# Kernel optimization log

Measured on AMD Instinct MI355X. Metric: run time of the kernel, lower is better.

Reference implementation:

```python
import jax, jax.numpy as jnp
import numpy as np

B, S, D, N, L, V = 2, 512, 1024, 4096, 4, 32000
EPS = 1e-5

def ternarize(w):
    # BitNet b1.58-style: scale = mean |w|, quantize to {-1,0,1}, rescale.
    s = jnp.mean(jnp.abs(w)) + 1e-8
    return s * jnp.round(jnp.clip(w / s, -1.0, 1.0))

def tern_ste(w):
    # straight-through estimator (faithful to ternary training)
    return w + jax.lax.stop_gradient(ternarize(w) - w)

def layer_norm(x, g, b):
    mu = jnp.mean(x, axis=-1, keepdims=True)
    var = jnp.var(x, axis=-1, keepdims=True)
    return (x - mu) * jax.lax.rsqrt(var + EPS) * g + b

def setup_inputs() -> dict:
    key = jax.random.key(0)
    ks = jax.random.split(key, 20)
    sc = lambda d: 1.0 / np.sqrt(d)
    inp = {
        'input_ids': jax.random.randint(ks[0], (B, S), 0, V, dtype=jnp.int32),
        'emb':       jax.random.normal(ks[1], (V, D), jnp.float32) * 0.02,
        'pos_emb':   jax.random.normal(ks[2], (S, D), jnp.float32) * 0.02,
        'gru_wih':   jax.random.normal(ks[3], (3 * D, D), jnp.float32) * sc(D),
        'gru_whh':   jax.random.normal(ks[4], (3 * D, D), jnp.float32) * sc(D),
        'gru_bih':   jnp.zeros((3 * D,), jnp.float32),
        'gru_bhh':   jnp.zeros((3 * D,), jnp.float32),
        'syn_w':     jax.random.normal(ks[5], (L, N, D), jnp.float32) * sc(D),
        'syn_b':     jnp.zeros((L, N), jnp.float32),
        'out_w':     jax.random.normal(ks[6], (L, D, N), jnp.float32) * sc(N),
        'out_b':     jnp.zeros((L, D), jnp.float32),
        'ln_g':      jnp.ones((L, D), jnp.float32),
        'ln_b':      jnp.zeros((L, D), jnp.float32),
        'on_g':      jnp.ones((D,), jnp.float32),
        'on_b':      jnp.zeros((D,), jnp.float32),
        'head_w':    jax.random.normal(ks[7], (V, D), jnp.float32) * sc(D),
        'head_b':    jnp.zeros((V,), jnp.float32),
    }
    return inp

def gru(x, wih, whh, bih, bhh):
    # x: [B,S,D] -> [B,S,D], torch nn.GRU semantics, h0 = 0
    # Precompute input projections for all timesteps: [B,S,3D]
    gi_all = jnp.einsum('bsd,ed->bse', x, wih) + bih
    def step(h, gi):
        gh = h @ whh.T + bhh
        ir, iz, inn = jnp.split(gi, 3, axis=-1)
        hr, hz, hn = jnp.split(gh, 3, axis=-1)
        r = jax.nn.sigmoid(ir + hr)
        z = jax.nn.sigmoid(iz + hz)
        n = jnp.tanh(inn + r * hn)
        h_new = (1.0 - z) * n + z * h
        return h_new, h_new
    h0 = jnp.zeros((x.shape[0], whh.shape[1]), x.dtype)
    _, hs = jax.lax.scan(step, h0, jnp.swapaxes(gi_all, 0, 1))
    return jnp.swapaxes(hs, 0, 1)

def reference(input_ids, emb, pos_emb, gru_wih, gru_whh, gru_bih, gru_bhh,
              syn_w, syn_b, out_w, out_b, ln_g, ln_b, on_g, on_b,
              head_w, head_b):
    # Ternary embedding lookup
    x = tern_ste(emb)[input_ids]                       # [B,S,D]
    x = x + pos_emb[None, :x.shape[1], :]
    x = gru(x, gru_wih, gru_whh, gru_bih, gru_bhh)
    for l in range(L):
        residual = x
        hidden = jax.nn.relu(jnp.einsum('bsd,nd->bsn', x, tern_ste(syn_w[l])) + syn_b[l])
        out = jnp.einsum('bsn,dn->bsd', hidden, tern_ste(out_w[l])) + out_b[l]
        x = layer_norm(residual + out, ln_g[l], ln_b[l])
    x = layer_norm(x, on_g, on_b)
    logits = jnp.einsum('bsd,vd->bsv', x, tern_ste(head_w)) + head_b  # [B,S,V]
    return logits
```

## Files before the change

kernel.cpp:

```cpp
#include <hip/hip_runtime.h>
#include <hip/hip_bf16.h>
#include <cstdint>
#include <cstddef>

#define Dm 1024
#define Sm 512
#define Bm 2
#define Nm 4096
#define Lm 4
#define Vm 32000

typedef __attribute__((ext_vector_type(8))) short short8;
typedef __attribute__((ext_vector_type(4))) float floatx4;

__device__ __forceinline__ unsigned short f2b(float f){
  union { float f; unsigned u; } v; v.f = f;
  unsigned r = (v.u + 0x7fffu + ((v.u >> 16) & 1u)) >> 16;
  return (unsigned short)r;
}

__device__ __forceinline__ float tern_thresh(double s64){
  float T = (float)(s64 * 0.5);
  if ((double)T > s64 * 0.5) T = __uint_as_float(__float_as_uint(T) - 1u);
  return T;
}

__global__ __launch_bounds__(256) void absum_part_kernel(
    const float* __restrict__ x, long n4, double* __restrict__ part)
{
  long i = (long)blockIdx.x * blockDim.x + threadIdx.x;
  long stride = (long)gridDim.x * blockDim.x;
  double s = 0.0;
  for (; i < n4; i += stride){
    float4 v = ((const float4*)x)[i];
    s += (double)fabsf(v.x) + (double)fabsf(v.y)
       + (double)fabsf(v.z) + (double)fabsf(v.w);
  }
  #pragma unroll
  for (int off = 32; off; off >>= 1) s += __shfl_down(s, off, 64);
  __shared__ double wsum[4];
  int lane = threadIdx.x & 63, wv = threadIdx.x >> 6;
  if (lane == 0) wsum[wv] = s;
  __syncthreads();
  if (threadIdx.x == 0) part[blockIdx.x] = wsum[0]+wsum[1]+wsum[2]+wsum[3];
}

__global__ __launch_bounds__(256) void absum_final_kernel(
    const double* __restrict__ part, double* __restrict__ scales)
{
  const double* p = part + (size_t)blockIdx.x * 512;
  int tid = threadIdx.x;
  double s = p[tid] + p[tid + 256];
  #pragma unroll
  for (int off = 32; off; off >>= 1) s += __shfl_down(s, off, 64);
  __shared__ double wsum[4];
  int lane = tid & 63, wv = tid >> 6;
  if (lane == 0) wsum[wv] = s;
  __syncthreads();
  if (tid == 0) scales[blockIdx.x] = wsum[0]+wsum[1]+wsum[2]+wsum[3];
}

__global__ __launch_bounds__(256) void pack_kernel(
    const float* __restrict__ src, unsigned short* __restrict__ dst, long n4,
    const double* __restrict__ ssum, double cnt)
{
  float T = 0.f;
  bool tern = (ssum != nullptr);
  if (tern){
    double s64 = ssum[0] / cnt + 1e-8;
    T = tern_thresh(s64);
  }
  long i = (long)blockIdx.x * blockDim.x + threadIdx.x;
  long stride = (long)gridDim.x * blockDim.x;
  for (; i < n4; i += stride){
    float4 v = ((const float4*)src)[i];
    ushort4 u;
    if (tern){
      u.x = (v.x > T) ? 0x3F80 : ((v.x < -T) ? 0xBF80 : 0);
      u.y = (v.y > T) ? 0x3F80 : ((v.y < -T) ? 0xBF80 : 0);
      u.z = (v.z > T) ? 0x3F80 : ((v.z < -T) ? 0xBF80 : 0);
      u.w = (v.w > T) ? 0x3F80 : ((v.w < -T) ? 0xBF80 : 0);
    } else {
      u.x = f2b(v.x); u.y = f2b(v.y); u.z = f2b(v.z); u.w = f2b(v.w);
    }
    ((ushort4*)dst)[i] = u;
  }
}

__global__ __launch_bounds__(256) void embed_kernel(
    const int* __restrict__ ids, const float* __restrict__ emb,
    const float* __restrict__ pos, const double* __restrict__ ssum,
    unsigned short* __restrict__ xb)
{
  int row = blockIdx.x;
  int sp  = row & (Sm - 1);
  int id  = ids[row];
  double s64 = ssum[0] / ((double)Vm * (double)Dm) + 1e-8;
  float s = (float)s64;
  float T = tern_thresh(s64);
  int d = threadIdx.x * 4;
  float4 wv = *(const float4*)(emb + (size_t)id * Dm + d);
  float4 pv = *(const float4*)(pos + (size_t)sp * Dm + d);
  float q0 = (wv.x > T) ? 1.f : ((wv.x < -T) ? -1.f : 0.f);
  float q1 = (wv.y > T) ? 1.f : ((wv.y < -T) ? -1.f : 0.f);
  float q2 = (wv.z > T) ? 1.f : ((wv.z < -T) ? -1.f : 0.f);
  float q3 = (wv.w > T) ? 1.f : ((wv.w < -T) ? -1.f : 0.f);
  float y0 = s * q0 + pv.x;
  float y1 = s * q1 + pv.y;
  float y2 = s * q2 + pv.z;
  float y3 = s * q3 + pv.w;
  ushort4 u = make_ushort4(f2b(y0), f2b(y1), f2b(y2), f2b(y3));
  *(ushort4*)(xb + (size_t)row * Dm + d) = u;
}

template<int WM>
__global__ __launch_bounds__(256) void gemm_t(
    const unsigned short* __restrict__ A, const void* __restrict__ Wp,
    const float* __restrict__ bias, const double* __restrict__ ssum, double cnt,
    int relu, float* __restrict__ outf, unsigned short* __restrict__ outb,
    int M, int N, int K)
{
  __shared__ unsigned short As[128][40];
  __shared__ unsigned short Bs[128][40];
  int tid = threadIdx.x;
  int wave = tid >> 6, lane = tid & 63;
  int wm = wave >> 1, wn = wave & 1;
  int bm = blockIdx.y, bn = blockIdx.x;

  float s = 1.f, T = 0.f;
  if (ssum){
    double s64 = ssum[0] / cnt + 1e-8;
    s = (float)s64;
    T = tern_thresh(s64);
  }

  int arow = tid >> 1, achunk = tid & 1;
  const unsigned short* Ag = A + (size_t)(bm * 128 + arow) * K + achunk * 16;
  const float* Wg32 = (const float*)Wp + (size_t)(bn * 128 + arow) * K + achunk * 16;
  const unsigned short* Wg16 = (const unsigned short*)Wp + (size_t)(bn * 128 + arow) * K + achunk * 16;

  floatx4 acc[4][4];
  #pragma unroll
  for (int i = 0; i < 4; i++)
    #pragma unroll
    for (int j = 0; j < 4; j++)
      acc[i][j] = (floatx4){0.f, 0.f, 0.f, 0.f};

  for (int k0 = 0; k0 < K; k0 += 32){
    __syncthreads();
    uint4 a0 = *(const uint4*)(Ag + k0);
    uint4 a1 = *(const uint4*)(Ag + k0 + 8);
    *(uint4*)&As[arow][achunk * 16]     = a0;
    *(uint4*)&As[arow][achunk * 16 + 8] = a1;
    if (WM == 2){
      uint4 b0 = *(const uint4*)(Wg16 + k0);
      uint4 b1 = *(const uint4*)(Wg16 + k0 + 8);
      *(uint4*)&Bs[arow][achunk * 16]     = b0;
      *(uint4*)&Bs[arow][achunk * 16 + 8] = b1;
    } else {
      unsigned short tmp[16];
      #pragma unroll
      for (int q = 0; q < 4; q++){
        float4 wv = *(const float4*)(Wg32 + k0 + q * 4);
        if (WM == 1){
          tmp[q*4+0] = (wv.x > T) ? 0x3F80 : ((wv.x < -T) ? 0xBF80 : 0);
          tmp[q*4+1] = (wv.y > T) ? 0x3F80 : ((wv.y < -T) ? 0xBF80 : 0);
          tmp[q*4+2] = (wv.z > T) ? 0x3F80 : ((wv.z < -T) ? 0xBF80 : 0);
          tmp[q*4+3] = (wv.w > T) ? 0x3F80 : ((wv.w < -T) ? 0xBF80 : 0);
        } else {
          tmp[q*4+0] = f2b(wv.x); tmp[q*4+1] = f2b(wv.y);
          tmp[q*4+2] = f2b(wv.z); tmp[q*4+3] = f2b(wv.w);
        }
      }
      *(uint4*)&Bs[arow][achunk * 16]     = *(uint4*)&tmp[0];
      *(uint4*)&Bs[arow][achunk * 16 + 8] = *(uint4*)&tmp[8];
    }
    __syncthreads();

    int kq = lane >> 4, mr = lane & 15;
    short8 af[4], bf[4];
    #pragma unroll
    for (int i = 0; i < 4; i++) af[i] = *(const short8*)&As[wm*64 + i*16 + mr][kq*8];
    #pragma unroll
    for (int j = 0; j < 4; j++) bf[j] = *(const short8*)&Bs[wn*64 + j*16 + mr][kq*8];
    #pragma unroll
    for (int i = 0; i < 4; i++)
      #pragma unroll
      for (int j = 0; j < 4; j++)
        acc[i][j] = __builtin_amdgcn_mfma_f32_16x16x32_bf16(af[i], bf[j], acc[i][j], 0, 0, 0);
  }

  int cr = lane >> 4, cc = lane & 15;
  #pragma unroll
  for (int j = 0; j < 4; j++){
    int col = bn * 128 + wn * 64 + j * 16 + cc;
    float bv = bias ? bias[col] : 0.f;
    #pragma unroll
    for (int i = 0; i < 4; i++){
      #pragma unroll
      for (int r = 0; r < 4; r++){
        int row = bm * 128 + wm * 64 + i * 16 + cr * 4 + r;
        float v = acc[i][j][r] * s + bv;
        if (relu) v = fmaxf(v, 0.f);
        size_t idx = (size_t)row * N + col;
        if (outf) outf[idx] = v;
        if (outb) outb[idx] = f2b(v);
      }
    }
  }
}

template<int WM>
__global__ __launch_bounds__(512) void gemm256_t(
    const unsigned short* __restrict__ A, const void* __restrict__ Wp,
    const float* __restrict__ bias, const double* __restrict__ ssum, double cnt,
    int relu, float* __restrict__ outf, unsigned short* __restrict__ outb,
    int M, int N, int K)
{
  __shared__ unsigned short As[256][40];
  __shared__ unsigned short Bs[128][40];
  int tid = threadIdx.x;
  int wave = tid >> 6, lane = tid & 63;
  int wm = wave >> 1, wn = wave & 1;
  int bm = blockIdx.y, bn = blockIdx.x;

  float s = 1.f, T = 0.f;
  if (ssum){
    double s64 = ssum[0] / cnt + 1e-8;
    s = (float)s64;
    T = tern_thresh(s64);
  }

  int arow = tid >> 1, achunk = tid & 1;
  int wrow = tid >> 2, wchunk = tid & 3;
  const unsigned short* Ag = A + (size_t)(bm * 256 + arow) * K + achunk * 16;
  const float* Wg32 = (const float*)Wp + (size_t)(bn * 128 + wrow) * K + wchunk * 8;
  const unsigned short* Wg16 = (const unsigned short*)Wp + (size_t)(bn * 128 + wrow) * K + wchunk * 8;

  floatx4 acc[4][4];
  #pragma unroll
  for (int i = 0; i < 4; i++)
    #pragma unroll
    for (int j = 0; j < 4; j++)
      acc[i][j] = (floatx4){0.f, 0.f, 0.f, 0.f};

  for (int k0 = 0; k0 < K; k0 += 32){
    __syncthreads();
    uint4 a0 = *(const uint4*)(Ag + k0);
    uint4 a1 = *(const uint4*)(Ag + k0 + 8);
    *(uint4*)&As[arow][achunk * 16]     = a0;
    *(uint4*)&As[arow][achunk * 16 + 8] = a1;
    if (WM == 2){
      uint4 b0 = *(const uint4*)(Wg16 + k0);
      *(uint4*)&Bs[wrow][wchunk * 8] = b0;
    } else {
      unsigned short tmp[8];
      float4 w0 = *(const float4*)(Wg32 + k0);
      float4 w1 = *(const float4*)(Wg32 + k0 + 4);
      if (WM == 1){
        tmp[0] = (w0.x > T) ? 0x3F80 : ((w0.x < -T) ? 0xBF80 : 0);
        tmp[1] = (w0.y > T) ? 0x3F80 : ((w0.y < -T) ? 0xBF80 : 0);
        tmp[2] = (w0.z > T) ? 0x3F80 : ((w0.z < -T) ? 0xBF80 : 0);
        tmp[3] = (w0.w > T) ? 0x3F80 : ((w0.w < -T) ? 0xBF80 : 0);
        tmp[4] = (w1.x > T) ? 0x3F80 : ((w1.x < -T) ? 0xBF80 : 0);
        tmp[5] = (w1.y > T) ? 0x3F80 : ((w1.y < -T) ? 0xBF80 : 0);
        tmp[6] = (w1.z > T) ? 0x3F80 : ((w1.z < -T) ? 0xBF80 : 0);
        tmp[7] = (w1.w > T) ? 0x3F80 : ((w1.w < -T) ? 0xBF80 : 0);
      } else {
        tmp[0] = f2b(w0.x); tmp[1] = f2b(w0.y); tmp[2] = f2b(w0.z); tmp[3] = f2b(w0.w);
        tmp[4] = f2b(w1.x); tmp[5] = f2b(w1.y); tmp[6] = f2b(w1.z); tmp[7] = f2b(w1.w);
      }
      *(uint2*)&Bs[wrow][wchunk * 8]     = *(uint2*)&tmp[0];
      *(uint2*)&Bs[wrow][wchunk * 8 + 4] = *(uint2*)&tmp[4];
    }
    __syncthreads();

    int kq = lane >> 4, mr = lane & 15;
    short8 af[4], bf[4];
    #pragma unroll
    for (int i = 0; i < 4; i++) af[i] = *(const short8*)&As[wm*64 + i*16 + mr][kq*8];
    #pragma unroll
    for (int j = 0; j < 4; j++) bf[j] = *(const short8*)&Bs[wn*64 + j*16 + mr][kq*8];
    #pragma unroll
    for (int i = 0; i < 4; i++)
      #pragma unroll
      for (int j = 0; j < 4; j++)
        acc[i][j] = __builtin_amdgcn_mfma_f32_16x16x32_bf16(af[i], bf[j], acc[i][j], 0, 0, 0);
  }

  int cr = lane >> 4, cc = lane & 15;
  #pragma unroll
  for (int j = 0; j < 4; j++){
    int col = bn * 128 + wn * 64 + j * 16 + cc;
    float bv = bias ? bias[col] : 0.f;
    #pragma unroll
    for (int i = 0; i < 4; i++){
      #pragma unroll
      for (int r = 0; r < 4; r++){
        int row = bm * 256 + wm * 64 + i * 16 + cr * 4 + r;
        float v = acc[i][j][r] * s + bv;
        if (relu) v = fmaxf(v, 0.f);
        size_t idx = (size_t)row * N + col;
        if (outf) outf[idx] = v;
        if (outb) outb[idx] = f2b(v);
      }
    }
  }
}

__global__ __launch_bounds__(512) void gru_kernel(
    const float* __restrict__ gi, const float* __restrict__ whh, const float* __restrict__ bhh,
    unsigned long long* __restrict__ hbuf,
    float* __restrict__ hs, unsigned short* __restrict__ hsb)
{
  __shared__ __align__(16) float lds_h[2][Dm];
  __shared__ float lds_gh[24];
  int w = blockIdx.x, tid = threadIdx.x;
  int bb = w & 1, slice = w >> 1;
  int d0 = slice * 8;
  int o = tid >> 4, c = tid & 15;
  bool active = (o < 24);
  int g = o >> 3, dl = o & 7;
  int wrow = g * Dm + d0 + dl;
  float4 wr0 = {0,0,0,0}, wr1 = wr0, wr2 = wr0, wr3 = wr0,
         wr4 = wr0, wr5 = wr0, wr6 = wr0, wr7 = wr0,
         wr8 = wr0, wr9 = wr0, wr10 = wr0, wr11 = wr0,
         wr12 = wr0, wr13 = wr0, wr14 = wr0, wr15 = wr0;
  if (active){
    const float* wsrc = whh + (size_t)wrow * Dm + c * 4;
    wr0  = *(const float4*)(wsrc +  0*64);  wr1  = *(const float4*)(wsrc +  1*64);
    wr2  = *(const float4*)(wsrc +  2*64);  wr3  = *(const float4*)(wsrc +  3*64);
    wr4  = *(const float4*)(wsrc +  4*64);  wr5  = *(const float4*)(wsrc +  5*64);
    wr6  = *(const float4*)(wsrc +  6*64);  wr7  = *(const float4*)(wsrc +  7*64);
    wr8  = *(const float4*)(wsrc +  8*64);  wr9  = *(const float4*)(wsrc +  9*64);
    wr10 = *(const float4*)(wsrc + 10*64);  wr11 = *(const float4*)(wsrc + 11*64);
    wr12 = *(const float4*)(wsrc + 12*64);  wr13 = *(const float4*)(wsrc + 13*64);
    wr14 = *(const float4*)(wsrc + 14*64);  wr15 = *(const float4*)(wsrc + 15*64);
  }
  float bhval = (active && c == 0) ? bhh[wrow] : 0.f;

  int gidx = tid * 2;
  bool self = ((tid >> 2) == slice);
  int dd = tid;
  int dth = d0 + (tid & 7);
  float pir = 0.f, piz = 0.f, pin = 0.f;
  if (tid < 8){
    const float* girow = gi + (size_t)bb * Sm * (3 * Dm);
    pir = girow[dth]; piz = girow[Dm + dth]; pin = girow[2*Dm + dth];
  }

  for (int t = 0; t < Sm; t++){
    float* lh = lds_h[t & 1];
    if (!self || t == 0){
      const unsigned long long* hsrc = hbuf + (size_t)(t & 1) * 2048 + bb * 1024 + gidx;
      unsigned long long e0, e1;
      int spins = 0;
      for (;;){
        e0 = __hip_atomic_load(hsrc + 0, __ATOMIC_RELAXED, __HIP_MEMORY_SCOPE_AGENT);
        e1 = __hip_atomic_load(hsrc + 1, __ATOMIC_RELAXED, __HIP_MEMORY_SCOPE_AGENT);
        if (((unsigned)(e0 >> 32) == (unsigned)t) &&
            ((unsigned)(e1 >> 32) == (unsigned)t)) break;
        __builtin_amdgcn_s_sleep(2);
        if (++spins > (1 << 16)) break;
      }
      lh[gidx + 0] = __uint_as_float((unsigned)e0);
      lh[gidx + 1] = __uint_as_float((unsigned)e1);
    }
    __syncthreads();
    float acc = 0.f;
    if (active){
      const float* hb = lh + c * 4;
      float4 hv;
      #define GDOT(J, W) hv = *(const float4*)(hb + (J)*64); \
          acc += W.x*hv.x + W.y*hv.y + W.z*hv.z + W.w*hv.w;
      GDOT(0,wr0)  GDOT(1,wr1)  GDOT(2,wr2)  GDOT(3,wr3)
      GDOT(4,wr4)  GDOT(5,wr5)  GDOT(6,wr6)  GDOT(7,wr7)
      GDOT(8,wr8)  GDOT(9,wr9)  GDOT(10,wr10) GDOT(11,wr11)
      GDOT(12,wr12) GDOT(13,wr13) GDOT(14,wr14) GDOT(15,wr15)
      #undef GDOT
    }
    #pragma unroll
    for (int off = 8; off; off >>= 1) acc += __shfl_xor(acc, off, 16);
    if (active && c == 0) lds_gh[o] = acc + bhval;
    __syncthreads();
    if (tid < 8){
      float gr = lds_gh[dd];
      float gz = lds_gh[8 + dd];
      float gn = lds_gh[16 + dd];
      float hv = lh[dth];
      float rr = 1.f / (1.f + expf(-(pir + gr)));
      float zz = 1.f / (1.f + expf(-(piz + gz)));
      float nn = tanhf(pin + rr * gn);
      float hnew = (1.f - zz) * nn + zz * hv;
      unsigned long long pack =
          ((unsigned long long)(unsigned)(t + 1) << 32) | (unsigned long long)__float_as_uint(hnew);
      __hip_atomic_store(hbuf + (size_t)((t + 1) & 1) * 2048 + bb * 1024 + dth, pack,
                         __ATOMIC_RELAXED, __HIP_MEMORY_SCOPE_AGENT);
      lds_h[(t + 1) & 1][dth] = hnew;
      if (t + 1 < Sm){
        const float* girow = gi + ((size_t)bb * Sm + (t+1)) * (3 * Dm);
        pir = girow[dth]; piz = girow[Dm + dth]; pin = girow[2*Dm + dth];
      }
      size_t oi = ((size_t)bb * Sm + t) * Dm + dth;
      hs[oi]  = hnew;
      hsb[oi] = f2b(hnew);
    }
  }
}

__global__ __launch_bounds__(256) void ln_kernel(
    float* __restrict__ resid, const float* __restrict__ addv,
    const float* __restrict__ g, const float* __restrict__ b,
    float* __restrict__ outf, unsigned short* __restrict__ outb)
{
  int row = blockIdx.x;
  int d = threadIdx.x * 4;
  size_t base = (size_t)row * Dm + d;
  float4 v = *(float4*)(resid + base);
  if (addv){
    float4 a = *(const float4*)(addv + base);
    v.x += a.x; v.y += a.y; v.z += a.z; v.w += a.w;
  }
  float sum = v.x + v.y + v.z + v.w;
  float sq  = v.x*v.x + v.y*v.y + v.z*v.z + v.w*v.w;
  #pragma unroll
  for (int off = 32; off; off >>= 1){
    sum += __shfl_down(sum, off, 64);
    sq  += __shfl_down(sq,  off, 64);
  }
  __shared__ float red[4][2];
  __shared__ float bc[2];
  int lane = threadIdx.x & 63, wv = threadIdx.x >> 6;
  if (lane == 0){ red[wv][0] = sum; red[wv][1] = sq; }
  __syncthreads();
  if (threadIdx.x == 0){
    float st = red[0][0] + red[1][0] + red[2][0] + red[3][0];
    float qt = red[0][1] + red[1][1] + red[2][1] + red[3][1];
    float mu = st * (1.f / Dm);
    float var = qt * (1.f / Dm) - mu * mu;
    bc[0] = mu; bc[1] = rsqrtf(var + 1e-5f);
  }
  __syncthreads();
  float mu = bc[0], rs = bc[1];
  float4 gv = *(const float4*)(g + d);
  float4 bv = *(const float4*)(b + d);
  float4 y;
  y.x = (v.x - mu) * rs * gv.x + bv.x;
  y.y = (v.y - mu) * rs * gv.y + bv.y;
  y.z = (v.z - mu) * rs * gv.z + bv.z;
  y.w = (v.w - mu) * rs * gv.w + bv.w;
  if (outf) *(float4*)(outf + base) = y;
  if (outb){
    ushort4 u = make_ushort4(f2b(y.x), f2b(y.y), f2b(y.z), f2b(y.w));
    *(ushort4*)(outb + base) = u;
  }
}

extern "C" void kernel_launch(void* const* d_in, const int* in_sizes, int n_in,
                              void* d_out, int out_size, void* d_ws, size_t ws_size,
                              hipStream_t stream)
{
  const int*   ids    = (const int*)  d_in[0];
  const float* emb    = (const float*)d_in[1];
  const float* pos    = (const float*)d_in[2];
  const float* wih    = (const float*)d_in[3];
  const float* whh    = (const float*)d_in[4];
  const float* bih    = (const float*)d_in[5];
  const float* bhh    = (const float*)d_in[6];
  const float* syn_w  = (const float*)d_in[7];
  const float* syn_b  = (const float*)d_in[8];
  const float* out_w  = (const float*)d_in[9];
  const float* out_b  = (const float*)d_in[10];
  const float* ln_g   = (const float*)d_in[11];
  const float* ln_b   = (const float*)d_in[12];
  const float* on_g   = (const float*)d_in[13];
  const float* on_b   = (const float*)d_in[14];
  const float* head_w = (const float*)d_in[15];
  const float* head_b = (const float*)d_in[16];
  float* logits = (float*)d_out;

  char* ws = (char*)d_ws;
  double*             scales = (double*)ws;
  unsigned long long* hbuf   = (unsigned long long*)(ws + 4096);
  double*             parts  = (double*)(ws + 36864);
  unsigned short*     xb     = (unsigned short*)(ws + 131072);
  float*              hs     = (float*)(ws + ((size_t)4  << 20));
  unsigned short*     hidden = (unsigned short*)(ws + ((size_t)12 << 20));
  float*              outbuf = (float*)(ws + ((size_t)20 << 20));
  float*              gi     = (float*)(ws + ((size_t)24 << 20));
  unsigned short*     wih_b  = (unsigned short*)(ws + ((size_t)36 << 20));
  unsigned short*     syn_bk = (unsigned short*)(ws + ((size_t)42 << 20));
  unsigned short*     out_bk = (unsigned short*)(ws + ((size_t)74 << 20));
  unsigned short*     head_bk= (unsigned short*)(ws + ((size_t)106 << 20));
  const size_t NEED = ((size_t)106 << 20) + (size_t)Vm * Dm * 2;
  const bool packed = (ws_size >= NEED);

  hipMemsetAsync(d_ws, 0, 36864, stream);

  {
    long n;
    n = (long)Vm * Dm;
    absum_part_kernel<<<512, 256, 0, stream>>>(emb, n / 4, parts + 0 * 512);
    for (int l = 0; l < Lm; l++){
      n = (long)Nm * Dm;
      absum_part_kernel<<<512, 256, 0, stream>>>(syn_w + (size_t)l * Nm * Dm, n / 4, parts + (size_t)(1 + l) * 512);
      absum_part_kernel<<<512, 256, 0, stream>>>(out_w + (size_t)l * Dm * Nm, n / 4, parts + (size_t)(5 + l) * 512);
    }
    n = (long)Vm * Dm;
    absum_part_kernel<<<512, 256, 0, stream>>>(head_w, n / 4, parts + 9 * 512);
    absum_final_kernel<<<10, 256, 0, stream>>>(parts, scales);
  }

  const double cnt_nd = (double)Nm * (double)Dm;
  const double cnt_vd = (double)Vm * (double)Dm;

  if (packed){
    pack_kernel<<<1024, 256, 0, stream>>>(wih, wih_b, (long)(3*Dm)*Dm/4, nullptr, 0.0);
    for (int l = 0; l < Lm; l++){
      pack_kernel<<<1024, 256, 0, stream>>>(syn_w + (size_t)l*Nm*Dm, syn_bk + (size_t)l*Nm*Dm,
                                            (long)Nm*Dm/4, scales + 1 + l, cnt_nd);
      pack_kernel<<<1024, 256, 0, stream>>>(out_w + (size_t)l*Dm*Nm, out_bk + (size_t)l*Dm*Nm,
                                            (long)Nm*Dm/4, scales + 5 + l, cnt_nd);
    }
    pack_kernel<<<2048, 256, 0, stream>>>(head_w, head_bk, (long)Vm*Dm/4, scales + 9, cnt_vd);
  }

  embed_kernel<<<1024, 256, 0, stream>>>(ids, emb, pos, scales, xb);

  if (packed)
    gemm_t<2><<<dim3(3072/128, 1024/128), 256, 0, stream>>>(
        xb, wih_b, bih, nullptr, 0.0, 0, gi, nullptr, 1024, 3072, 1024);
  else
    gemm_t<0><<<dim3(3072/128, 1024/128), 256, 0, stream>>>(
        xb, wih, bih, nullptr, 0.0, 0, gi, nullptr, 1024, 3072, 1024);

  gru_kernel<<<256, 512, 0, stream>>>(gi, whh, bhh, hbuf, hs, xb);

  for (int l = 0; l < Lm; l++){
    if (packed){
      gemm_t<2><<<dim3(4096/128, 1024/128), 256, 0, stream>>>(
          xb, syn_bk + (size_t)l * Nm * Dm, syn_b + (size_t)l * Nm,
          scales + 1 + l, cnt_nd, 1, nullptr, hidden, 1024, 4096, 1024);
      gemm_t<2><<<dim3(1024/128, 1024/128), 256, 0, stream>>>(
          hidden, out_bk + (size_t)l * Dm * Nm, out_b + (size_t)l * Dm,
          scales + 5 + l, cnt_nd, 0, outbuf, nullptr, 1024, 1024, 4096);
    } else {
      gemm_t<1><<<dim3(4096/128, 1024/128), 256, 0, stream>>>(
          xb, syn_w + (size_t)l * Nm * Dm, syn_b + (size_t)l * Nm,
          scales + 1 + l, cnt_nd, 1, nullptr, hidden, 1024, 4096, 1024);
      gemm_t<1><<<dim3(1024/128, 1024/128), 256, 0, stream>>>(
          hidden, out_w + (size_t)l * Dm * Nm, out_b + (size_t)l * Dm,
          scales + 5 + l, cnt_nd, 0, outbuf, nullptr, 1024, 1024, 4096);
    }
    ln_kernel<<<1024, 256, 0, stream>>>(hs, outbuf, ln_g + (size_t)l * Dm, ln_b + (size_t)l * Dm, hs, xb);
  }
  ln_kernel<<<1024, 256, 0, stream>>>(hs, nullptr, on_g, on_b, nullptr, xb);

  if (packed)
    gemm256_t<2><<<dim3(32000/128, 1024/256), 512, 0, stream>>>(
        xb, head_bk, head_b, scales + 9, cnt_vd, 0, logits, nullptr, 1024, 32000, 1024);
  else
    gemm256_t<1><<<dim3(32000/128, 1024/256), 512, 0, stream>>>(
        xb, head_w, head_b, scales + 9, cnt_vd, 0, logits, nullptr, 1024, 32000, 1024);
}
```

Baseline: 2.453 ms.

## Split-K the out-projection GEMM and batch weight scale/pack launches

The N->D projection GEMM had only 64 blocks on a long K dimension, so it is split four ways along K. The partial sums are written into the idle gi buffer and reduced inside the layer-norm kernel. The per-tensor abs-sum and ternary pack kernels are merged into single launches indexed by blockIdx.y, which cuts launch count. In exchange, the split adds extra partial-sum memory traffic and relies on gi being dead after the GRU.

```diff
diff --git a/kernel.cpp b/kernel.cpp
--- a/kernel.cpp
+++ b/kernel.cpp
@@ -25,9 +25,14 @@
   return T;
 }
 
-__global__ __launch_bounds__(256) void absum_part_kernel(
-    const float* __restrict__ x, long n4, double* __restrict__ part)
-{
+struct AbsumArgs { const float* src[10]; long n4[10]; };
+
+__global__ __launch_bounds__(256) void absum_all_kernel(
+    AbsumArgs a, double* __restrict__ parts)
+{
+  int slot = blockIdx.y;
+  const float* x = a.src[slot];
+  long n4 = a.n4[slot];
   long i = (long)blockIdx.x * blockDim.x + threadIdx.x;
   long stride = (long)gridDim.x * blockDim.x;
   double s = 0.0;
@@ -42,7 +47,8 @@
   int lane = threadIdx.x & 63, wv = threadIdx.x >> 6;
   if (lane == 0) wsum[wv] = s;
   __syncthreads();
-  if (threadIdx.x == 0) part[blockIdx.x] = wsum[0]+wsum[1]+wsum[2]+wsum[3];
+  if (threadIdx.x == 0)
+    parts[(size_t)slot * 512 + blockIdx.x] = wsum[0]+wsum[1]+wsum[2]+wsum[3];
 }
 
 __global__ __launch_bounds__(256) void absum_final_kernel(
@@ -60,14 +66,22 @@
   if (tid == 0) scales[blockIdx.x] = wsum[0]+wsum[1]+wsum[2]+wsum[3];
 }
 
-__global__ __launch_bounds__(256) void pack_kernel(
-    const float* __restrict__ src, unsigned short* __restrict__ dst, long n4,
-    const double* __restrict__ ssum, double cnt)
-{
+struct PackArgs {
+  const float* src[10]; unsigned short* dst[10];
+  long n4[10]; int sidx[10]; double cnt[10];
+};
+
+__global__ __launch_bounds__(256) void pack_all_kernel(
+    PackArgs a, const double* __restrict__ scales)
+{
+  int slot = blockIdx.y;
+  const float* src = a.src[slot];
+  unsigned short* dst = a.dst[slot];
+  long n4 = a.n4[slot];
+  bool tern = (a.sidx[slot] >= 0);
   float T = 0.f;
-  bool tern = (ssum != nullptr);
   if (tern){
-    double s64 = ssum[0] / cnt + 1e-8;
+    double s64 = scales[a.sidx[slot]] / a.cnt[slot] + 1e-8;
     T = tern_thresh(s64);
   }
   long i = (long)blockIdx.x * blockDim.x + threadIdx.x;
@@ -205,6 +219,96 @@
         size_t idx = (size_t)row * N + col;
         if (outf) outf[idx] = v;
         if (outb) outb[idx] = f2b(v);
+      }
+    }
+  }
+}
+
+template<int WM>
+__global__ __launch_bounds__(256) void gemm_ks_t(
+    const unsigned short* __restrict__ A, const void* __restrict__ Wp,
+    const float* __restrict__ bias, const double* __restrict__ ssum, double cnt,
+    float* __restrict__ p0, float* __restrict__ pext,
+    int M, int N, int K, int Klen)
+{
+  __shared__ unsigned short As[128][40];
+  __shared__ unsigned short Bs[128][40];
+  int tid = threadIdx.x;
+  int wave = tid >> 6, lane = tid & 63;
+  int wm = wave >> 1, wn = wave & 1;
+  int bm = blockIdx.y, bn = blockIdx.x, z = blockIdx.z;
+
+  float s = 1.f, T = 0.f;
+  if (ssum){
+    double s64 = ssum[0] / cnt + 1e-8;
+    s = (float)s64;
+    T = tern_thresh(s64);
+  }
+
+  int arow = tid >> 1, achunk = tid & 1;
+  int kbase = z * Klen;
+  const unsigned short* Ag = A + (size_t)(bm * 128 + arow) * K + kbase + achunk * 16;
+  const float* Wg32 = (const float*)Wp + (size_t)(bn * 128 + arow) * K + kbase + achunk * 16;
+  const unsigned short* Wg16 = (const unsigned short*)Wp + (size_t)(bn * 128 + arow) * K + kbase + achunk * 16;
+
+  floatx4 acc[4][4];
+  #pragma unroll
+  for (int i = 0; i < 4; i++)
+    #pragma unroll
+    for (int j = 0; j < 4; j++)
+      acc[i][j] = (floatx4){0.f, 0.f, 0.f, 0.f};
+
+  for (int k0 = 0; k0 < Klen; k0 += 32){
+    __syncthreads();
+    uint4 a0 = *(const uint4*)(Ag + k0);
+    uint4 a1 = *(const uint4*)(Ag + k0 + 8);
+    *(uint4*)&As[arow][achunk * 16]     = a0;
+    *(uint4*)&As[arow][achunk * 16 + 8] = a1;
+    if (WM == 2){
+      uint4 b0 = *(const uint4*)(Wg16 + k0);
+      uint4 b1 = *(const uint4*)(Wg16 + k0 + 8);
+      *(uint4*)&Bs[arow][achunk * 16]     = b0;
+      *(uint4*)&Bs[arow][achunk * 16 + 8] = b1;
+    } else {
+      unsigned short tmp[16];
+      #pragma unroll
+      for (int q = 0; q < 4; q++){
+        float4 wv = *(const float4*)(Wg32 + k0 + q * 4);
+        tmp[q*4+0] = (wv.x > T) ? 0x3F80 : ((wv.x < -T) ? 0xBF80 : 0);
+        tmp[q*4+1] = (wv.y > T) ? 0x3F80 : ((wv.y < -T) ? 0xBF80 : 0);
+        tmp[q*4+2] = (wv.z > T) ? 0x3F80 : ((wv.z < -T) ? 0xBF80 : 0);
+        tmp[q*4+3] = (wv.w > T) ? 0x3F80 : ((wv.w < -T) ? 0xBF80 : 0);
+      }
+      *(uint4*)&Bs[arow][achunk * 16]     = *(uint4*)&tmp[0];
+      *(uint4*)&Bs[arow][achunk * 16 + 8] = *(uint4*)&tmp[8];
+    }
+    __syncthreads();
+
+    int kq = lane >> 4, mr = lane & 15;
+    short8 af[4], bf[4];
+    #pragma unroll
+    for (int i = 0; i < 4; i++) af[i] = *(const short8*)&As[wm*64 + i*16 + mr][kq*8];
+    #pragma unroll
+    for (int j = 0; j < 4; j++) bf[j] = *(const short8*)&Bs[wn*64 + j*16 + mr][kq*8];
+    #pragma unroll
+    for (int i = 0; i < 4; i++)
+      #pragma unroll
+      for (int j = 0; j < 4; j++)
+        acc[i][j] = __builtin_amdgcn_mfma_f32_16x16x32_bf16(af[i], bf[j], acc[i][j], 0, 0, 0);
+  }
+
+  float* outp = (z == 0) ? p0 : pext + (size_t)(z - 1) * M * N;
+  int cr = lane >> 4, cc = lane & 15;
+  #pragma unroll
+  for (int j = 0; j < 4; j++){
+    int col = bn * 128 + wn * 64 + j * 16 + cc;
+    float bv = (z == 0 && bias) ? bias[col] : 0.f;
+    #pragma unroll
+    for (int i = 0; i < 4; i++){
+      #pragma unroll
+      for (int r = 0; r < 4; r++){
+        int row = bm * 128 + wm * 64 + i * 16 + cr * 4 + r;
+        outp[(size_t)row * N + col] = acc[i][j][r] * s + bv;
       }
     }
   }
@@ -409,7 +513,8 @@
 }
 
 __global__ __launch_bounds__(256) void ln_kernel(
-    float* __restrict__ resid, const float* __restrict__ addv,
+    float* __restrict__ resid, const float* __restrict__ p0,
+    const float* __restrict__ pext,
     const float* __restrict__ g, const float* __restrict__ b,
     float* __restrict__ outf, unsigned short* __restrict__ outb)
 {
@@ -417,9 +522,17 @@
   int d = threadIdx.x * 4;
   size_t base = (size_t)row * Dm + d;
   float4 v = *(float4*)(resid + base);
-  if (addv){
-    float4 a = *(const float4*)(addv + base);
+  if (p0){
+    float4 a = *(const float4*)(p0 + base);
     v.x += a.x; v.y += a.y; v.z += a.z; v.w += a.w;
+  }
+  if (pext){
+    const size_t stride = (size_t)1024 * Dm;
+    #pragma unroll
+    for (int e = 0; e < 3; e++){
+      float4 a = *(const float4*)(pext + e * stride + base);
+      v.x += a.x; v.y += a.y; v.z += a.z; v.w += a.w;
+    }
   }
   float sum = v.x + v.y + v.z + v.w;
   float sq  = v.x*v.x + v.y*v.y + v.z*v.z + v.w*v.w;
@@ -497,32 +610,32 @@
 
   hipMemsetAsync(d_ws, 0, 36864, stream);
 
-  {
-    long n;
-    n = (long)Vm * Dm;
-    absum_part_kernel<<<512, 256, 0, stream>>>(emb, n / 4, parts + 0 * 512);
-    for (int l = 0; l < Lm; l++){
-      n = (long)Nm * Dm;
-      absum_part_kernel<<<512, 256, 0, stream>>>(syn_w + (size_t)l * Nm * Dm, n / 4, parts + (size_t)(1 + l) * 512);
-      absum_part_kernel<<<512, 256, 0, stream>>>(out_w + (size_t)l * Dm * Nm, n / 4, parts + (size_t)(5 + l) * 512);
-    }
-    n = (long)Vm * Dm;
-    absum_part_kernel<<<512, 256, 0, stream>>>(head_w, n / 4, parts + 9 * 512);
-    absum_final_kernel<<<10, 256, 0, stream>>>(parts, scales);
-  }
-
   const double cnt_nd = (double)Nm * (double)Dm;
   const double cnt_vd = (double)Vm * (double)Dm;
 
+  {
+    AbsumArgs aa;
+    aa.src[0] = emb;    aa.n4[0] = (long)Vm * Dm / 4;
+    for (int l = 0; l < Lm; l++){
+      aa.src[1 + l] = syn_w + (size_t)l * Nm * Dm; aa.n4[1 + l] = (long)Nm * Dm / 4;
+      aa.src[5 + l] = out_w + (size_t)l * Dm * Nm; aa.n4[5 + l] = (long)Nm * Dm / 4;
+    }
+    aa.src[9] = head_w; aa.n4[9] = (long)Vm * Dm / 4;
+    absum_all_kernel<<<dim3(512, 10), 256, 0, stream>>>(aa, parts);
+    absum_final_kernel<<<10, 256, 0, stream>>>(parts, scales);
+  }
+
   if (packed){
-    pack_kernel<<<1024, 256, 0, stream>>>(wih, wih_b, (long)(3*Dm)*Dm/4, nullptr, 0.0);
+    PackArgs pa;
+    pa.src[0] = wih;  pa.dst[0] = wih_b;  pa.n4[0] = (long)(3*Dm)*Dm/4; pa.sidx[0] = -1; pa.cnt[0] = 1.0;
     for (int l = 0; l < Lm; l++){
-      pack_kernel<<<1024, 256, 0, stream>>>(syn_w + (size_t)l*Nm*Dm, syn_bk + (size_t)l*Nm*Dm,
-                                            (long)Nm*Dm/4, scales + 1 + l, cnt_nd);
-      pack_kernel<<<1024, 256, 0, stream>>>(out_w + (size_t)l*Dm*Nm, out_bk + (size_t)l*Dm*Nm,
-                                            (long)Nm*Dm/4, scales + 5 + l, cnt_nd);
-    }
-    pack_kernel<<<2048, 256, 0, stream>>>(head_w, head_bk, (long)Vm*Dm/4, scales + 9, cnt_vd);
+      pa.src[1+l] = syn_w + (size_t)l*Nm*Dm; pa.dst[1+l] = syn_bk + (size_t)l*Nm*Dm;
+      pa.n4[1+l] = (long)Nm*Dm/4; pa.sidx[1+l] = 1 + l; pa.cnt[1+l] = cnt_nd;
+      pa.src[5+l] = out_w + (size_t)l*Dm*Nm; pa.dst[5+l] = out_bk + (size_t)l*Dm*Nm;
+      pa.n4[5+l] = (long)Nm*Dm/4; pa.sidx[5+l] = 5 + l; pa.cnt[5+l] = cnt_nd;
+    }
+    pa.src[9] = head_w; pa.dst[9] = head_bk; pa.n4[9] = (long)Vm*Dm/4; pa.sidx[9] = 9; pa.cnt[9] = cnt_vd;
+    pack_all_kernel<<<dim3(512, 10), 256, 0, stream>>>(pa, scales);
   }
 
   embed_kernel<<<1024, 256, 0, stream>>>(ids, emb, pos, scales, xb);
@@ -537,24 +650,26 @@
   gru_kernel<<<256, 512, 0, stream>>>(gi, whh, bhh, hbuf, hs, xb);
 
   for (int l = 0; l < Lm; l++){
-    if (packed){
+    if (packed)
       gemm_t<2><<<dim3(4096/128, 1024/128), 256, 0, stream>>>(
           xb, syn_bk + (size_t)l * Nm * Dm, syn_b + (size_t)l * Nm,
           scales + 1 + l, cnt_nd, 1, nullptr, hidden, 1024, 4096, 1024);
-      gemm_t<2><<<dim3(1024/128, 1024/128), 256, 0, stream>>>(
-          hidden, out_bk + (size_t)l * Dm * Nm, out_b + (size_t)l * Dm,
-          scales + 5 + l, cnt_nd, 0, outbuf, nullptr, 1024, 1024, 4096);
-    } else {
+    else
       gemm_t<1><<<dim3(4096/128, 1024/128), 256, 0, stream>>>(
           xb, syn_w + (size_t)l * Nm * Dm, syn_b + (size_t)l * Nm,
           scales + 1 + l, cnt_nd, 1, nullptr, hidden, 1024, 4096, 1024);
-      gemm_t<1><<<dim3(1024/128, 1024/128), 256, 0, stream>>>(
+    if (packed)
+      gemm_ks_t<2><<<dim3(1024/128, 1024/128, 4), 256, 0, stream>>>(
+          hidden, out_bk + (size_t)l * Dm * Nm, out_b + (size_t)l * Dm,
+          scales + 5 + l, cnt_nd, outbuf, gi, 1024, 1024, 4096, 1024);
+    else
+      gemm_ks_t<1><<<dim3(1024/128, 1024/128, 4), 256, 0, stream>>>(
           hidden, out_w + (size_t)l * Dm * Nm, out_b + (size_t)l * Dm,
-          scales + 5 + l, cnt_nd, 0, outbuf, nullptr, 1024, 1024, 4096);
-    }
-    ln_kernel<<<1024, 256, 0, stream>>>(hs, outbuf, ln_g + (size_t)l * Dm, ln_b + (size_t)l * Dm, hs, xb);
-  }
-  ln_kernel<<<1024, 256, 0, stream>>>(hs, nullptr, on_g, on_b, nullptr, xb);
+          scales + 5 + l, cnt_nd, outbuf, gi, 1024, 1024, 4096, 1024);
+    ln_kernel<<<1024, 256, 0, stream>>>(hs, outbuf, gi,
+        ln_g + (size_t)l * Dm, ln_b + (size_t)l * Dm, hs, xb);
+  }
+  ln_kernel<<<1024, 256, 0, stream>>>(hs, nullptr, nullptr, on_g, on_b, nullptr, xb);
 
   if (packed)
     gemm256_t<2><<<dim3(32000/128, 1024/256), 512, 0, stream>>>(
```

Result: faster. 2.112 ms (-13.9%).
